# Optimization experiments

Measured on AMD Instinct MI355X. Metric: run time of the kernel, lower is better.

## Reference

```python
import jax, jax.numpy as jnp
import numpy as np

B, R, C, S, K = 8, 16, 512, 512, 64
GAMMA = 0.99
DPP = 1 * (8192 // 512)  # n_device * n_block_per_update = 16


def setup_inputs() -> dict:
    key = jax.random.key(0)
    k1, k2, k3 = jax.random.split(key, 3)
    vecs = jax.random.normal(k1, (B, R, C, K), dtype=jnp.float32)
    c_sum = jax.random.normal(k2, (S, K), dtype=jnp.float32)
    # realistic EMA usage counts, strictly positive
    c_count = jax.random.uniform(k3, (S,), dtype=jnp.float32) * 100.0 + 1.0
    return {"vecs": vecs, "c_sum": c_sum, "c_count": c_count}


def reference(vecs, c_sum, c_count):
    sg = jax.lax.stop_gradient
    st = lambda x: x - sg(x)

    # codebook from EMA stats (stop-gradient, as in _get_codebook)
    c = sg(c_sum / jnp.clip(c_count[:, None], 0.01))  # [S,K]

    # get_shortcodes: squared distances via three contractions (no cdist materialized beyond [B,R,C,S])
    diffs2 = (jnp.sum(jnp.square(vecs), axis=-1)[..., None]
              - 2.0 * jnp.einsum('brck,sk->brcs', vecs, c)
              + jnp.sum(jnp.square(c), axis=-1)[None, None, None, :])  # [B,R,C,S]
    z = jnp.argmin(diffs2, axis=-1).astype(jnp.int32)  # [B,R,C]
    errs2 = jax.nn.relu(jnp.min(diffs2, axis=-1))      # [B,R,C]

    # get_codewords: gather codewords (equivalent to take_along_axis in original)
    cz = jnp.take(c, z, axis=0)  # [B,R,C,K]

    # straight-through estimator
    vecs_hat = sg(cz) + st(vecs)

    # commitment loss (head_type == 'shga': no extra sum over axis 1)
    l_commit = jnp.mean(errs2)

    # codebook EMA-target loss; targets only ever appear under stop_gradient
    vflat = sg(vecs).reshape(-1, K)
    zflat = z.reshape(-1)
    c_sum_hat = DPP * jax.ops.segment_sum(vflat, zflat, num_segments=S)          # [S,K]
    c_count_hat = DPP * jax.ops.segment_sum(jnp.ones_like(zflat, jnp.float32), zflat, num_segments=S)  # [S]
    c_sum_tgt = (1.0 - GAMMA) * c_sum_hat + GAMMA * sg(c_sum)
    c_count_tgt = (1.0 - GAMMA) * c_count_hat + GAMMA * sg(c_count)
    l_codebook = (jnp.sum(sg(c_sum - c_sum_tgt) * st(c_sum))
                  + jnp.sum(sg(c_count - c_count_tgt) * st(c_count)))

    return (vecs_hat, z, l_commit, l_codebook, errs2)
```

## Files before the change

### kernel.cpp

```cpp
#include <hip/hip_runtime.h>

#define NVEC 65536
#define KDIM 64
#define SDIM 512

#define Z_OFF       4194304
#define LCOMMIT_OFF 4259840
#define LCODE_OFF   4259841
#define E_OFF       4259842

typedef _Float16 half8    __attribute__((ext_vector_type(8)));
typedef float    floatx16 __attribute__((ext_vector_type(16)));


__global__ void vq_prep(const float* __restrict__ c_sum,
                        const float* __restrict__ c_count,
                        float* __restrict__ c32,
                        float* __restrict__ cnorm,
                        _Float16* __restrict__ cbf16,
                        float* __restrict__ out) {
    int s = blockIdx.x;
    int k = threadIdx.x;
    float cnt = c_count[s];
    float inv = 1.0f / fmaxf(cnt, 0.01f);
    float x = c_sum[s * KDIM + k] * inv;
    c32[s * KDIM + k] = x;
    float sq = x * x;
    #pragma unroll
    for (int off = 32; off > 0; off >>= 1)
        sq += __shfl_down(sq, off);
    if (k == 0) cnorm[s] = sq;

    __shared__ _Float16 hb[64], lb[64];
    _Float16 hi = (_Float16)x;
    float hiF = (float)hi;
    _Float16 lo = (_Float16)(x - hiF);
    hb[k] = hi; lb[k] = lo;
    __syncthreads();
    if (k < 16) {
        int p  = k >> 3;
        int qh = k & 7;
        int k0 = (qh >> 1) * 16 + (qh & 1) * 8;
        const _Float16* srcb = (p ? lb : hb) + k0;
        half8 v;
        #pragma unroll
        for (int j = 0; j < 8; ++j) v[j] = srcb[j];
        size_t chunk = ((size_t)(s >> 5) * 16 + p * 8 + qh) * 32 + (s & 31);
        *(half8*)(cbf16 + chunk * 8) = v;
    }
    if (s == 0 && k == 0) {
        out[LCOMMIT_OFF] = 0.0f;
        out[LCODE_OFF]   = 0.0f;
    }
}

__global__ __launch_bounds__(256, 2) void vq_main(const float* __restrict__ vecs,
                                                  const _Float16* __restrict__ cbf16,
                                                  const float* __restrict__ c32,
                                                  const float* __restrict__ cnorm,
                                                  float* __restrict__ out) {
    __shared__ float cnL[512];
    __shared__ float vnL[4][32];
    __shared__ int   zL[4][32];
    __shared__ float esumL[8];

    const int tx   = threadIdx.x;
    const int lane = tx & 63;
    const int w    = tx >> 6;
    const int col  = lane & 31;
    const int h    = lane >> 5;
    const int wvec = (int)blockIdx.x * 128 + w * 32;

    cnL[tx]       = cnorm[tx];
    cnL[tx + 256] = cnorm[tx + 256];

    half8 ahi[4], alo[4];
    float vnp = 0.0f;
    const float* arow = vecs + (size_t)(wvec + col) * KDIM + h * 8;
    #pragma unroll
    for (int q = 0; q < 4; ++q) {
        float4 x0 = *(const float4*)(arow + q * 16);
        float4 x1 = *(const float4*)(arow + q * 16 + 4);
        #define CVT(X, J) { float xx = (X); _Float16 hi5 = (_Float16)xx; \
                            float hf = (float)hi5; ahi[q][J] = hi5; \
                            alo[q][J] = (_Float16)(xx - hf); vnp += xx * xx; }
        CVT(x0.x, 0) CVT(x0.y, 1) CVT(x0.z, 2) CVT(x0.w, 3)
        CVT(x1.x, 4) CVT(x1.y, 5) CVT(x1.z, 6) CVT(x1.w, 7)
        #undef CVT
    }
    vnp += __shfl_xor(vnp, 32);
    if (h == 0) vnL[w][col] = vnp;

    __syncthreads();

    float bm[16];
    int   bi[16];
    #pragma unroll
    for (int r = 0; r < 16; ++r) { bm[r] = -3.4e38f; bi[r] = 0; }

    for (int t = 0; t < 4; ++t) {
        const _Float16* bt = cbf16 + (size_t)t * 16384 + lane * 8;
        #pragma unroll
        for (int sub = 0; sub < 4; ++sub) {
            const _Float16* bb = bt + sub * 4096;
            float ci = -0.5f * cnL[t * 128 + sub * 32 + col];
            floatx16 a0, a1;
            #pragma unroll
            for (int r = 0; r < 16; ++r) { a0[r] = ci; a1[r] = 0.0f; }
            #pragma unroll
            for (int q = 0; q < 4; ++q) {
                half8 bh = *(const half8*)(bb + q * 512);
                half8 bl = *(const half8*)(bb + 2048 + q * 512);
                a0 = __builtin_amdgcn_mfma_f32_32x32x16_f16(ahi[q], bh, a0, 0, 0, 0);
                a1 = __builtin_amdgcn_mfma_f32_32x32x16_f16(alo[q], bh, a1, 0, 0, 0);
                a1 = __builtin_amdgcn_mfma_f32_32x32x16_f16(ahi[q], bl, a1, 0, 0, 0);
            }
            int n = t * 128 + sub * 32 + col;
            #pragma unroll
            for (int r = 0; r < 16; ++r) {
                float m = a0[r] + a1[r];
                if (m > bm[r]) { bm[r] = m; bi[r] = n; }
            }
        }
    }

    #pragma unroll
    for (int r = 0; r < 16; ++r) {
        float v = bm[r]; int i = bi[r];
        #pragma unroll
        for (int off = 16; off > 0; off >>= 1) {
            float ov = __shfl_xor(v, off);
            int   oi = __shfl_xor(i, off);
            if (ov > v || (ov == v && oi < i)) { v = ov; i = oi; }
        }
        bm[r] = v; bi[r] = i;
    }

    if (col == 0) {
        float esum = 0.0f;
        #pragma unroll
        for (int r = 0; r < 16; ++r) {
            int row = (r & 3) + 8 * (r >> 2) + 4 * h;
            int vid = wvec + row;
            float err = fmaxf(vnL[w][row] - 2.0f * bm[r], 0.0f);
            out[Z_OFF + vid] = (float)bi[r];
            out[E_OFF + vid] = err;
            zL[w][row] = bi[r];
            esum += err;
        }
        esumL[w * 2 + h] = esum;
    }

    #pragma unroll
    for (int it = 0; it < 8; ++it) {
        int row = it * 4 + (lane >> 4);
        int c4  = lane & 15;
        int z   = zL[w][row];
        float4 val = *(const float4*)(c32 + (size_t)z * KDIM + c4 * 4);
        *(float4*)(out + (size_t)(wvec + row) * KDIM + c4 * 4) = val;
    }

    __syncthreads();
    if (tx == 0) {
        float tot = esumL[0] + esumL[1] + esumL[2] + esumL[3]
                  + esumL[4] + esumL[5] + esumL[6] + esumL[7];
        atomicAdd(out + LCOMMIT_OFF, tot * (1.0f / (float)NVEC));
    }
}

extern "C" void kernel_launch(void* const* d_in, const int* in_sizes, int n_in,
                              void* d_out, int out_size, void* d_ws, size_t ws_size,
                              hipStream_t stream) {
    const float* vecs    = (const float*)d_in[0];
    const float* c_sum   = (const float*)d_in[1];
    const float* c_count = (const float*)d_in[2];
    float* out = (float*)d_out;

    float*    c32   = (float*)d_ws;
    float*    cnorm = c32 + SDIM * KDIM;
    _Float16* cbf16 = (_Float16*)(cnorm + SDIM);

    vq_prep<<<SDIM, KDIM, 0, stream>>>(c_sum, c_count, c32, cnorm, cbf16, out);
    vq_main<<<NVEC / 128, 256, 0, stream>>>(vecs, cbf16, c32, cnorm, out);
}
```

Baseline: 109.4 us.

## Use single-wave blocks with register norms and a separate loss reduction kernel

Restructures the main kernel from 4-wave blocks over 128 vectors into one-wave blocks over 32 vectors (2048 blocks). Codebook norms now live in registers and vector norms are shuffled between lanes instead of going through LDS, which removes the block barrier. The three MFMAs per K-chunk now feed one accumulator instead of two. The commit-loss atomicAdd is replaced by per-block partial sums that a new single-block reduce kernel adds up, at the cost of a third kernel launch and a serial MFMA accumulator chain.

```diff
diff --git a/kernel.cpp b/kernel.cpp
--- a/kernel.cpp
+++ b/kernel.cpp
@@ -17,8 +17,7 @@
                         const float* __restrict__ c_count,
                         float* __restrict__ c32,
                         float* __restrict__ cnorm,
-                        _Float16* __restrict__ cbf16,
-                        float* __restrict__ out) {
+                        _Float16* __restrict__ cbf16) {
     int s = blockIdx.x;
     int k = threadIdx.x;
     float cnt = c_count[s];
@@ -48,31 +47,24 @@
         size_t chunk = ((size_t)(s >> 5) * 16 + p * 8 + qh) * 32 + (s & 31);
         *(half8*)(cbf16 + chunk * 8) = v;
     }
-    if (s == 0 && k == 0) {
-        out[LCOMMIT_OFF] = 0.0f;
-        out[LCODE_OFF]   = 0.0f;
-    }
 }
 
-__global__ __launch_bounds__(256, 2) void vq_main(const float* __restrict__ vecs,
-                                                  const _Float16* __restrict__ cbf16,
-                                                  const float* __restrict__ c32,
-                                                  const float* __restrict__ cnorm,
-                                                  float* __restrict__ out) {
-    __shared__ float cnL[512];
-    __shared__ float vnL[4][32];
-    __shared__ int   zL[4][32];
-    __shared__ float esumL[8];
+__global__ __launch_bounds__(64, 3) void vq_main(const float* __restrict__ vecs,
+                                                 const _Float16* __restrict__ cbf16,
+                                                 const float* __restrict__ c32,
+                                                 const float* __restrict__ cnorm,
+                                                 float* __restrict__ out,
+                                                 float* __restrict__ partial) {
+    __shared__ int zL[32];
 
-    const int tx   = threadIdx.x;
-    const int lane = tx & 63;
-    const int w    = tx >> 6;
+    const int lane = threadIdx.x;
     const int col  = lane & 31;
     const int h    = lane >> 5;
-    const int wvec = (int)blockIdx.x * 128 + w * 32;
+    const int wvec = (int)blockIdx.x * 32;
 
-    cnL[tx]       = cnorm[tx];
-    cnL[tx + 256] = cnorm[tx + 256];
+    float cnr[16];
+    #pragma unroll
+    for (int j = 0; j < 16; ++j) cnr[j] = -0.5f * cnorm[j * 32 + col];
 
     half8 ahi[4], alo[4];
     float vnp = 0.0f;
@@ -89,38 +81,31 @@
         #undef CVT
     }
     vnp += __shfl_xor(vnp, 32);
-    if (h == 0) vnL[w][col] = vnp;
-
-    __syncthreads();
 
     float bm[16];
     int   bi[16];
     #pragma unroll
     for (int r = 0; r < 16; ++r) { bm[r] = -3.4e38f; bi[r] = 0; }
 
-    for (int t = 0; t < 4; ++t) {
-        const _Float16* bt = cbf16 + (size_t)t * 16384 + lane * 8;
+    #pragma unroll
+    for (int j = 0; j < 16; ++j) {
+        const _Float16* bb = cbf16 + (size_t)j * 4096 + lane * 8;
+        float ci = cnr[j];
+        floatx16 a;
         #pragma unroll
-        for (int sub = 0; sub < 4; ++sub) {
-            const _Float16* bb = bt + sub * 4096;
-            float ci = -0.5f * cnL[t * 128 + sub * 32 + col];
-            floatx16 a0, a1;
-            #pragma unroll
-            for (int r = 0; r < 16; ++r) { a0[r] = ci; a1[r] = 0.0f; }
-            #pragma unroll
-            for (int q = 0; q < 4; ++q) {
-                half8 bh = *(const half8*)(bb + q * 512);
-                half8 bl = *(const half8*)(bb + 2048 + q * 512);
-                a0 = __builtin_amdgcn_mfma_f32_32x32x16_f16(ahi[q], bh, a0, 0, 0, 0);
-                a1 = __builtin_amdgcn_mfma_f32_32x32x16_f16(alo[q], bh, a1, 0, 0, 0);
-                a1 = __builtin_amdgcn_mfma_f32_32x32x16_f16(ahi[q], bl, a1, 0, 0, 0);
-            }
-            int n = t * 128 + sub * 32 + col;
-            #pragma unroll
-            for (int r = 0; r < 16; ++r) {
-                float m = a0[r] + a1[r];
-                if (m > bm[r]) { bm[r] = m; bi[r] = n; }
-            }
+        for (int r = 0; r < 16; ++r) a[r] = ci;
+        #pragma unroll
+        for (int q = 0; q < 4; ++q) {
+            half8 bh = *(const half8*)(bb + q * 512);
+            half8 bl = *(const half8*)(bb + 2048 + q * 512);
+            a = __builtin_amdgcn_mfma_f32_32x32x16_f16(ahi[q], bh, a, 0, 0, 0);
+            a = __builtin_amdgcn_mfma_f32_32x32x16_f16(alo[q], bh, a, 0, 0, 0);
+            a = __builtin_amdgcn_mfma_f32_32x32x16_f16(ahi[q], bl, a, 0, 0, 0);
+        }
+        int n = j * 32 + col;
+        #pragma unroll
+        for (int r = 0; r < 16; ++r) {
+            if (a[r] > bm[r]) { bm[r] = a[r]; bi[r] = n; }
         }
     }
 
@@ -136,35 +121,54 @@
         bm[r] = v; bi[r] = i;
     }
 
+    float vnr[16];
+    #pragma unroll
+    for (int r = 0; r < 16; ++r) {
+        int row = (r & 3) + 8 * (r >> 2) + 4 * h;
+        vnr[r] = __shfl(vnp, row);
+    }
+
+    float esum = 0.0f;
     if (col == 0) {
-        float esum = 0.0f;
         #pragma unroll
         for (int r = 0; r < 16; ++r) {
             int row = (r & 3) + 8 * (r >> 2) + 4 * h;
             int vid = wvec + row;
-            float err = fmaxf(vnL[w][row] - 2.0f * bm[r], 0.0f);
+            float err = fmaxf(vnr[r] - 2.0f * bm[r], 0.0f);
             out[Z_OFF + vid] = (float)bi[r];
             out[E_OFF + vid] = err;
-            zL[w][row] = bi[r];
+            zL[row] = bi[r];
             esum += err;
         }
-        esumL[w * 2 + h] = esum;
     }
+    esum += __shfl_xor(esum, 32);
+    if (lane == 0) partial[blockIdx.x] = esum;
 
     #pragma unroll
     for (int it = 0; it < 8; ++it) {
         int row = it * 4 + (lane >> 4);
         int c4  = lane & 15;
-        int z   = zL[w][row];
+        int z   = zL[row];
         float4 val = *(const float4*)(c32 + (size_t)z * KDIM + c4 * 4);
         *(float4*)(out + (size_t)(wvec + row) * KDIM + c4 * 4) = val;
     }
+}
 
+__global__ void vq_reduce(const float* __restrict__ partial,
+                          float* __restrict__ out) {
+    __shared__ float ws[4];
+    int tx = threadIdx.x;
+    float s = 0.0f;
+    #pragma unroll
+    for (int j = 0; j < 8; ++j) s += partial[tx + j * 256];
+    #pragma unroll
+    for (int off = 32; off > 0; off >>= 1) s += __shfl_down(s, off);
+    if ((tx & 63) == 0) ws[tx >> 6] = s;
     __syncthreads();
     if (tx == 0) {
-        float tot = esumL[0] + esumL[1] + esumL[2] + esumL[3]
-                  + esumL[4] + esumL[5] + esumL[6] + esumL[7];
-        atomicAdd(out + LCOMMIT_OFF, tot * (1.0f / (float)NVEC));
+        float tot = ws[0] + ws[1] + ws[2] + ws[3];
+        out[LCOMMIT_OFF] = tot * (1.0f / (float)NVEC);
+        out[LCODE_OFF]   = 0.0f;
     }
 }
 
@@ -176,10 +180,12 @@
     const float* c_count = (const float*)d_in[2];
     float* out = (float*)d_out;
 
-    float*    c32   = (float*)d_ws;
-    float*    cnorm = c32 + SDIM * KDIM;
-    _Float16* cbf16 = (_Float16*)(cnorm + SDIM);
+    float*    c32     = (float*)d_ws;
+    float*    cnorm   = c32 + SDIM * KDIM;
+    _Float16* cbf16   = (_Float16*)(cnorm + SDIM);
+    float*    partial = (float*)(cbf16 + SDIM * KDIM * 2);
 
-    vq_prep<<<SDIM, KDIM, 0, stream>>>(c_sum, c_count, c32, cnorm, cbf16, out);
-    vq_main<<<NVEC / 128, 256, 0, stream>>>(vecs, cbf16, c32, cnorm, out);
+    vq_prep<<<SDIM, KDIM, 0, stream>>>(c_sum, c_count, c32, cnorm, cbf16);
+    vq_main<<<NVEC / 32, 64, 0, stream>>>(vecs, cbf16, c32, cnorm, out, partial);
+    vq_reduce<<<1, 256, 0, stream>>>(partial, out);
 }
```

Result: slower. 286.0 us (+161.3%).
